# Performance work log

Hardware: AMD Instinct MI355X
Metric: run time of the kernel (lower is better)

Reference implementation:

```python
import jax, jax.numpy as jnp
import numpy as np

# Mamba2 defaults (mamba_ssm): d_state=128, d_conv=4, expand=2, headdim=64, ngroups=1
NB, D_MODEL, D_STATE, D_CONV, HEADDIM = 2, 512, 128, 4, 64
D_INNER = 2 * D_MODEL                      # expand * d_model
NHEADS = D_INNER // HEADDIM                # 16
CONV_DIM = D_INNER + 2 * D_STATE           # x, B, C go through depthwise conv
D_IN_PROJ = 2 * D_INNER + 2 * D_STATE + NHEADS  # z, xBC, dt
VOCAB, LABEL, B, L = 32000, 1000, 2, 512


def setup_inputs() -> dict:
    key = jax.random.key(0)
    ks = jax.random.split(key, 8)
    nrm = lambda k, shape, s: jax.random.normal(k, shape, dtype=jnp.float32) * s
    tokens = jax.random.randint(ks[0], (B, L), 0, VOCAB)
    embedding = nrm(ks[1], (VOCAB, D_MODEL), 0.02)
    in_proj_w = nrm(ks[2], (NB, D_IN_PROJ, D_MODEL), D_MODEL ** -0.5)
    conv_w = nrm(ks[3], (NB, CONV_DIM, D_CONV), D_CONV ** -0.5)
    conv_b = jnp.zeros((NB, CONV_DIM), jnp.float32)
    # dt_bias = inverse-softplus of dt ~ logUniform[1e-3, 0.1] (Mamba2 init)
    dt = jnp.exp(jax.random.uniform(ks[4], (NB, NHEADS), minval=float(np.log(1e-3)), maxval=float(np.log(0.1))))
    dt_bias = dt + jnp.log(-jnp.expm1(-dt))
    A_log = jnp.log(jax.random.uniform(ks[5], (NB, NHEADS), minval=1.0, maxval=16.0))
    D = jnp.ones((NB, NHEADS), jnp.float32)
    rms_w = jnp.ones((NB, D_INNER), jnp.float32)
    out_proj_w = nrm(ks[6], (NB, D_MODEL, D_INNER), D_INNER ** -0.5)
    ln_w = jnp.ones((NB, D_MODEL), jnp.float32)
    ln_b = jnp.zeros((NB, D_MODEL), jnp.float32)
    head_w = nrm(ks[7], (LABEL, D_MODEL), D_MODEL ** -0.5)
    head_b = jnp.zeros((LABEL,), jnp.float32)
    return dict(tokens=tokens, embedding=embedding, in_proj_w=in_proj_w, conv_w=conv_w,
                conv_b=conv_b, dt_bias=dt_bias, A_log=A_log, D=D, rms_w=rms_w,
                out_proj_w=out_proj_w, ln_w=ln_w, ln_b=ln_b, head_w=head_w, head_b=head_b)


def _mamba2(u, Wi, cw, cb, dtb, Alog, Dv, rw, Wo):
    b, l, _ = u.shape
    zxbcdt = u @ Wi.T                                  # (b,l,D_IN_PROJ)
    z = zxbcdt[..., :D_INNER]
    xBC = zxbcdt[..., D_INNER:D_INNER + CONV_DIM]
    dt = jax.nn.softplus(zxbcdt[..., D_INNER + CONV_DIM:] + dtb)   # (b,l,h)
    # causal depthwise conv1d, kernel size D_CONV
    xp = jnp.pad(xBC, ((0, 0), (D_CONV - 1, 0), (0, 0)))
    xBC = sum(xp[:, k:k + l, :] * cw[:, k] for k in range(D_CONV)) + cb
    xBC = jax.nn.silu(xBC)
    xh = xBC[..., :D_INNER].reshape(b, l, NHEADS, HEADDIM)
    Bm = xBC[..., D_INNER:D_INNER + D_STATE]           # (b,l,n), ngroups=1
    Cm = xBC[..., D_INNER + D_STATE:]                  # (b,l,n)
    A = -jnp.exp(Alog)                                 # (h,)
    dA = jnp.exp(dt * A)                               # (b,l,h)

    def step(h, inp):
        dA_t, dt_t, x_t, B_t, C_t = inp                # (b,h),(b,h),(b,h,p),(b,n),(b,n)
        h = h * dA_t[:, :, None, None] + (dt_t[:, :, None] * x_t)[..., None] * B_t[:, None, None, :]
        return h, jnp.einsum('bhpn,bn->bhp', h, C_t)

    h0 = jnp.zeros((b, NHEADS, HEADDIM, D_STATE), u.dtype)
    inp = (jnp.swapaxes(dA, 0, 1), jnp.swapaxes(dt, 0, 1), jnp.swapaxes(xh, 0, 1),
           jnp.swapaxes(Bm, 0, 1), jnp.swapaxes(Cm, 0, 1))
    _, ys = jax.lax.scan(step, h0, inp)
    y = jnp.swapaxes(ys, 0, 1) + Dv[:, None] * xh      # (b,l,h,p)
    # gated RMSNorm (norm_before_gate=False): normalize y*silu(z)
    y = y.reshape(b, l, D_INNER) * jax.nn.silu(z)
    y = y * jax.lax.rsqrt(jnp.mean(y * y, -1, keepdims=True) + 1e-5) * rw
    return y @ Wo.T


def _layernorm(x, w, bias):
    mu = jnp.mean(x, -1, keepdims=True)
    xc = x - mu
    var = jnp.mean(xc * xc, -1, keepdims=True)
    return xc * jax.lax.rsqrt(var + 1e-5) * w + bias


def reference(tokens, embedding, in_proj_w, conv_w, conv_b, dt_bias, A_log, D,
              rms_w, out_proj_w, ln_w, ln_b, head_w, head_b):
    x = embedding[tokens]                              # (b,l,d)
    for i in range(NB):
        y = _mamba2(x, in_proj_w[i], conv_w[i], conv_b[i], dt_bias[i],
                    A_log[i], D[i], rms_w[i], out_proj_w[i])
        x = _layernorm(y + x, ln_w[i], ln_b[i])        # residual + LN (dropout=identity)
    return x @ head_w.T + head_b                        # (b,l,label)
```

## Files before the change

### kernel.cpp

```cpp
#include <hip/hip_runtime.h>

#define L_SEQ 512
#define BATCH 2
#define NROWS (BATCH*L_SEQ)
#define DMODEL 512
#define DINNER 1024
#define DSTATE 128
#define NHEADSM 16
#define CONVD 1280
#define DINPROJ 2320
#define QCH 32
#define NCH 16
#define WI_PAD 2368
#define WH_PAD 1024

#define W_CONVW 0
#define W_CONVB 10240
#define W_DTB   12800
#define W_ALOG  12832
#define W_DD    12864
#define W_RMSW  12896
#define W_LNW   14944
#define W_LNB   15968
#define W_HEADB 16992
#define O_X     18048
#define O_ZX    (O_X  + NROWS*DMODEL)
#define O_XC    (O_ZX + NROWS*DINPROJ)
#define O_DT    (O_XC + NROWS*CONVD)
#define O_Y     (O_DT + NROWS*NHEADSM)
#define O_O     (O_Y  + NROWS*DINNER)
#define O_LA    (O_O  + NROWS*DMODEL)
#define O_S     (O_LA + 16384)
#define O_UB    (O_S  + 4194304)
#define U_WI   0
#define U_WO   2424832
#define U_WH   3473408
#define U_XBF  3997696
#define U_YBF  4521984

#define NSMALL 17992
#define NPREPW (2*WI_PAD + 2*DMODEL + WH_PAD)

typedef __attribute__((ext_vector_type(8))) short short8;
typedef __attribute__((ext_vector_type(4))) float floatx4;

__device__ __forceinline__ float b2f(unsigned short h){ return __uint_as_float(((unsigned)h)<<16); }
__device__ __forceinline__ unsigned short f2b(float x){
  unsigned u = __float_as_uint(x);
  return (unsigned short)((u + 0x7fffu + ((u>>16)&1u)) >> 16);
}
__device__ __forceinline__ float loadIn(const void* p, long i, int f){
  return f ? b2f(((const unsigned short*)p)[i]) : ((const float*)p)[i];
}

__device__ __forceinline__ void gload16(const void* g, void* l){
  __builtin_amdgcn_global_load_lds((const __attribute__((address_space(1))) void*)g,
                                   (__attribute__((address_space(3))) void*)l, 16, 0, 0);
}

__global__ void k_detect(const unsigned* __restrict__ emb, int* __restrict__ flag){
  __shared__ int red[256];
  int t = threadIdx.x; int cnt = 0;
  for (int i = 0; i < 16; i++){
    unsigned w = emb[t*16 + i];
    unsigned e = (w >> 7) & 0xffu;
    cnt += (e >= 100 && e <= 126) ? 1 : 0;
  }
  red[t] = cnt; __syncthreads();
  if (t == 0){
    int s = 0;
    for (int i = 0; i < 256; i++) s += red[i];
    *flag = (s > 2048) ? 1 : 0;
  }
}

struct ConvArgs { const void* src[9]; int off[10]; };

__global__ void k_prep(ConvArgs a, const void* __restrict__ wi, const void* __restrict__ wo,
                       const void* __restrict__ wh, const int* __restrict__ tok,
                       const void* __restrict__ emb, const int* __restrict__ flag,
                       float* __restrict__ dstSmall,
                       unsigned short* __restrict__ WiB, unsigned short* __restrict__ WoB,
                       unsigned short* __restrict__ WhB,
                       float* __restrict__ x, unsigned short* __restrict__ xbf)
{
  int f = *flag;
  int blk = blockIdx.x;
  if (blk < 71){
    int i = blk*256 + threadIdx.x;
    if (i < a.off[9]){
      int s = 0;
      while (i >= a.off[s+1]) s++;
      dstSmall[i] = loadIn(a.src[s], i - a.off[s], f);
    }
    return;
  }
  blk -= 71;
  if (blk < NPREPW){
    int r = blk;
    const void* src = nullptr; unsigned short* dst; long sb = 0, db; int K; bool zero = false;
    if (r < 2*WI_PAD){
      int layer = r / WI_PAD, row = r % WI_PAD;
      K = DMODEL; dst = WiB; db = ((long)layer*WI_PAD + row)*DMODEL;
      if (row < DINPROJ){ src = wi; sb = ((long)layer*DINPROJ + row)*DMODEL; } else zero = true;
    } else if (r < 2*WI_PAD + 2*DMODEL){
      int rr = r - 2*WI_PAD;
      K = DINNER; dst = WoB; db = (long)rr*DINNER;
      src = wo; sb = db;
    } else {
      int row = r - 2*WI_PAD - 2*DMODEL;
      K = DMODEL; dst = WhB; db = (long)row*DMODEL;
      if (row < 1000){ src = wh; sb = db; } else zero = true;
    }
    for (int c = threadIdx.x; c < K; c += 256)
      dst[db + c] = zero ? (unsigned short)0
                         : (f ? ((const unsigned short*)src)[sb + c] : f2b(((const float*)src)[sb + c]));
    return;
  }
  int r = blk - NPREPW;
  long base = (long)tok[r] * DMODEL;
  for (int c = threadIdx.x; c < DMODEL; c += 256){
    float v = loadIn(emb, base + c, f);
    x[(long)r*DMODEL + c] = v;
    xbf[(long)r*DMODEL + c] = f ? ((const unsigned short*)emb)[base + c] : f2b(v);
  }
}

template<int BM, int BN>
__global__ __launch_bounds__(256) void k_mfma_nt(
    const unsigned short* __restrict__ A, const unsigned short* __restrict__ B,
    void* __restrict__ C, int M, int N, int K,
    const float* __restrict__ bias, const int* __restrict__ flag, int outDual)
{
  constexpr int MI = BM/32;
  constexpr int NI = BN/32;
  constexpr int CA = BM/32;
  constexpr int CB = BN/32;
  __shared__ __align__(16) unsigned short As[2][BM*64];
  __shared__ __align__(16) unsigned short Bs[2][BN*64];
  int f = *flag;
  int t = threadIdx.x;
  int w = t >> 6, lane = t & 63;
  int quad = lane >> 4, l16 = lane & 15;
  int m0 = blockIdx.y * BM, n0 = blockIdx.x * BN;
  int wm = (w & 1) * (BM/2), wn = (w >> 1) * (BN/2);
  floatx4 acc[MI][NI];
  #pragma unroll
  for (int mi = 0; mi < MI; mi++)
    #pragma unroll
    for (int ni = 0; ni < NI; ni++) acc[mi][ni] = (floatx4){0.f,0.f,0.f,0.f};

  const char* Ag = (const char*)A;
  const char* Bg = (const char*)B;
  long aOff[CA]; int aL[CA];
  #pragma unroll
  for (int j = 0; j < CA; j++){
    int i = (w*CA + j)*64 + lane;
    int r = i >> 3, g = (i & 7) ^ (r & 7);
    aOff[j] = ((long)(m0 + r)*K + g*8)*2;
    aL[j] = (w*CA + j)*1024;
  }
  long bOff[CB]; int bL[CB];
  #pragma unroll
  for (int j = 0; j < CB; j++){
    int i = (w*CB + j)*64 + lane;
    int r = i >> 3, g = (i & 7) ^ (r & 7);
    bOff[j] = ((long)(n0 + r)*K + g*8)*2;
    bL[j] = (w*CB + j)*1024;
  }

  const int NKI = K >> 6;
  #pragma unroll
  for (int j = 0; j < CA; j++) gload16(Ag + aOff[j], (char*)As[0] + aL[j]);
  #pragma unroll
  for (int j = 0; j < CB; j++) gload16(Bg + bOff[j], (char*)Bs[0] + bL[j]);
  asm volatile("s_waitcnt vmcnt(0)" ::: "memory");
  __syncthreads();

  for (int ki = 0; ki < NKI; ki++){
    int cur = ki & 1;
    if (ki + 1 < NKI){
      long kb = (long)(ki + 1)*128;
      #pragma unroll
      for (int j = 0; j < CA; j++) gload16(Ag + aOff[j] + kb, (char*)As[cur^1] + aL[j]);
      #pragma unroll
      for (int j = 0; j < CB; j++) gload16(Bg + bOff[j] + kb, (char*)Bs[cur^1] + bL[j]);
    }
    const unsigned short* Ac = As[cur];
    const unsigned short* Bc = Bs[cur];
    #pragma unroll
    for (int ks = 0; ks < 2; ks++){
      short8 af[MI], bfr[NI];
      #pragma unroll
      for (int mi = 0; mi < MI; mi++){
        int r = wm + mi*16 + l16;
        int pos = ((ks << 2) + quad) ^ (r & 7);
        af[mi] = *(const short8*)&Ac[r*64 + pos*8];
      }
      #pragma unroll
      for (int ni = 0; ni < NI; ni++){
        int r = wn + ni*16 + l16;
        int pos = ((ks << 2) + quad) ^ (r & 7);
        bfr[ni] = *(const short8*)&Bc[r*64 + pos*8];
      }
      #pragma unroll
      for (int mi = 0; mi < MI; mi++)
        #pragma unroll
        for (int ni = 0; ni < NI; ni++)
          acc[mi][ni] = __builtin_amdgcn_mfma_f32_16x16x32_bf16(af[mi], bfr[ni], acc[mi][ni], 0, 0, 0);
    }
    asm volatile("s_waitcnt vmcnt(0)" ::: "memory");
    __syncthreads();
  }
  #pragma unroll
  for (int mi = 0; mi < MI; mi++)
    #pragma unroll
    for (int ni = 0; ni < NI; ni++){
      int col = n0 + wn + ni*16 + l16;
      if (col >= N) continue;
      float bv = bias ? bias[col] : 0.f;
      #pragma unroll
      for (int rr = 0; rr < 4; rr++){
        int row = m0 + wm + mi*16 + (quad << 2) + rr;
        float v = acc[mi][ni][rr] + bv;
        long idx = (long)row*N + col;
        if (outDual && f) ((unsigned short*)C)[idx] = f2b(v);
        else              ((float*)C)[idx] = v;
      }
    }
}

__global__ __launch_bounds__(256) void k_conv_dt(
    const float* __restrict__ zx, const float* __restrict__ cw, const float* __restrict__ cb,
    const float* __restrict__ dtb, float* __restrict__ xc, float* __restrict__ dt)
{
  int r = blockIdx.x; int b = r >> 9, l = r & 511;
  int t = threadIdx.x;
  for (int c = t; c < CONVD; c += 256){
    float s = cb[c];
    #pragma unroll
    for (int k = 0; k < 4; k++){
      int pos = l - 3 + k;
      if (pos >= 0)
        s = fmaf(zx[(long)(b*L_SEQ + pos)*DINPROJ + DINNER + c], cw[c*4 + k], s);
    }
    xc[(long)r*CONVD + c] = s / (1.f + __expf(-s));
  }
  if (t < NHEADSM){
    float v = zx[(long)r*DINPROJ + DINNER + CONVD + t] + dtb[t];
    dt[r*NHEADSM + t] = (v > 20.f) ? v : log1pf(__expf(v));
  }
}

__global__ __launch_bounds__(256) void k_chunk1(
    const float* __restrict__ xc, const float* __restrict__ dtbuf,
    const float* __restrict__ alog, const float* __restrict__ dvec,
    float* __restrict__ S, float* __restrict__ LAb, float* __restrict__ y)
{
  int c = blockIdx.x, h = blockIdx.y, b = blockIdx.z;
  int t = threadIdx.x, w = t >> 6, lane = t & 63;
  int quad = lane >> 4, l16 = lane & 15;
  int l0 = c*QCH;
  __shared__ unsigned short XT[64*40];
  __shared__ unsigned short BTc[128*40];
  __shared__ unsigned short Bb[32*136];
  __shared__ unsigned short Cb[32*136];
  __shared__ unsigned short Gb[32*40];
  __shared__ float dtl[32], lal[32], coef[32];
  float A  = -__expf(alog[h]);
  float Dv = dvec[h];

  float xv[8];
  #pragma unroll
  for (int k = 0; k < 8; k++){
    int idx = t + k*256; int j = idx >> 6, p = idx & 63;
    xv[k] = xc[(long)(b*L_SEQ + l0 + j)*CONVD + h*64 + p];
  }
  float bv[16], cv[16];
  #pragma unroll
  for (int k = 0; k < 16; k++){
    int idx = t + k*256; int j = idx >> 7, n = idx & 127;
    long rb = (long)(b*L_SEQ + l0 + j)*CONVD + DINNER;
    bv[k] = xc[rb + n];
    cv[k] = xc[rb + DSTATE + n];
  }
  if (t < 32){
    float d = dtbuf[(b*L_SEQ + l0 + t)*NHEADSM + h];
    dtl[t] = d;
    float s = d;
    #pragma unroll
    for (int o = 1; o < 32; o <<= 1){
      float u = __shfl_up(s, o, 32);
      if (t >= o) s += u;
    }
    float la = s * A;
    lal[t] = la;
    float tot = __shfl(s, 31, 32) * A;
    coef[t] = __expf(tot - la) * d;
    LAb[(b*NHEADSM + h)*L_SEQ + l0 + t] = la;
  }
  __syncthreads();
  #pragma unroll
  for (int k = 0; k < 8; k++){
    int idx = t + k*256; int j = idx >> 6, p = idx & 63;
    XT[p*40 + j] = f2b(xv[k]);
  }
  #pragma unroll
  for (int k = 0; k < 16; k++){
    int idx = t + k*256; int j = idx >> 7, n = idx & 127;
    Bb[j*136 + n] = f2b(bv[k]);
    Cb[j*136 + n] = f2b(cv[k]);
    BTc[n*40 + j] = f2b(bv[k] * coef[j]);
  }
  __syncthreads();

  short8 afS = *(const short8*)&XT[(w*16 + l16)*40 + quad*8];
  floatx4 accS[8];
  #pragma unroll
  for (int nb = 0; nb < 8; nb++){
    short8 bfS = *(const short8*)&BTc[(nb*16 + l16)*40 + quad*8];
    accS[nb] = __builtin_amdgcn_mfma_f32_16x16x32_bf16(afS, bfS, (floatx4){0.f,0.f,0.f,0.f}, 0, 0, 0);
  }
  int ti = w & 1, tj = w >> 1;
  floatx4 accG = (floatx4){0.f,0.f,0.f,0.f};
  #pragma unroll
  for (int ks = 0; ks < 4; ks++){
    short8 ga = *(const short8*)&Cb[(ti*16 + l16)*136 + ks*32 + quad*8];
    short8 gb = *(const short8*)&Bb[(tj*16 + l16)*136 + ks*32 + quad*8];
    accG = __builtin_amdgcn_mfma_f32_16x16x32_bf16(ga, gb, accG, 0, 0, 0);
  }
  long sb = ((long)((b*NHEADSM + h)*NCH + c))*8192;
  #pragma unroll
  for (int nb = 0; nb < 8; nb++)
    #pragma unroll
    for (int rr = 0; rr < 4; rr++)
      S[sb + (w*16 + quad*4 + rr)*128 + nb*16 + l16] = accS[nb][rr];
  #pragma unroll
  for (int rr = 0; rr < 4; rr++){
    int i = ti*16 + quad*4 + rr, j = tj*16 + l16;
    float g = (j <= i) ? __expf(lal[i] - lal[j]) * dtl[j] * accG[rr] : 0.f;
    Gb[i*40 + j] = f2b(g);
  }
  __syncthreads();
  short8 ag = *(const short8*)&Gb[(ti*16 + l16)*40 + quad*8];
  #pragma unroll
  for (int s = 0; s < 2; s++){
    int pb = (w >> 1)*2 + s;
    short8 bx = *(const short8*)&XT[(pb*16 + l16)*40 + quad*8];
    floatx4 accY = __builtin_amdgcn_mfma_f32_16x16x32_bf16(ag, bx, (floatx4){0.f,0.f,0.f,0.f}, 0, 0, 0);
    #pragma unroll
    for (int rr = 0; rr < 4; rr++){
      int i = ti*16 + quad*4 + rr, p = pb*16 + l16;
      float xval = b2f(XT[p*40 + i]);
      y[(long)(b*L_SEQ + l0 + i)*DINNER + h*64 + p] = fmaf(Dv, xval, accY[rr]);
    }
  }
}

__global__ __launch_bounds__(256) void k_chunk2(
    float* __restrict__ S, const float* __restrict__ LAb)
{
  int bh = blockIdx.x >> 5;
  int e = ((blockIdx.x & 31) << 8) + threadIdx.x;
  long base = (long)bh*NCH*8192 + e;
  int laBase = bh*L_SEQ;
  float lam[NCH];
  #pragma unroll
  for (int c = 0; c < NCH; c++) lam[c] = __expf(LAb[laBase + c*QCH + QCH - 1]);
  float hr = 0.f;
  #pragma unroll
  for (int c = 0; c < NCH; c++){
    long off = base + (long)c*8192;
    float sv = S[off];
    S[off] = hr;
    hr = fmaf(hr, lam[c], sv);
  }
}

__global__ __launch_bounds__(256) void k_chunk3(
    const float* __restrict__ xc, const float* __restrict__ H,
    const float* __restrict__ LAb, float* __restrict__ y)
{
  int c = blockIdx.x, h = blockIdx.y, b = blockIdx.z;
  int t = threadIdx.x, w = t >> 6, lane = t & 63;
  int quad = lane >> 4, l16 = lane & 15;
  int l0 = c*QCH;
  __shared__ unsigned short Cb[32*136];
  __shared__ unsigned short Hhi[64*136];
  __shared__ unsigned short Hlo[64*136];
  __shared__ float el[32];
  if (t < 32) el[t] = __expf(LAb[(b*NHEADSM + h)*L_SEQ + l0 + t]);
  #pragma unroll
  for (int k = 0; k < 16; k++){
    int idx = t + k*256; int j = idx >> 7, n = idx & 127;
    Cb[j*136 + n] = f2b(xc[(long)(b*L_SEQ + l0 + j)*CONVD + DINNER + DSTATE + n]);
  }
  long hb = ((long)((b*NHEADSM + h)*NCH + c))*8192;
  #pragma unroll
  for (int k = 0; k < 32; k++){
    int idx = t + k*256; int p = idx >> 7, n = idx & 127;
    float v = H[hb + idx];
    unsigned short hi = f2b(v);
    Hhi[p*136 + n] = hi;
    Hlo[p*136 + n] = f2b(v - b2f(hi));
  }
  __syncthreads();
  int ti = w & 1;
  #pragma unroll
  for (int s = 0; s < 2; s++){
    int pb = (w >> 1)*2 + s;
    floatx4 acc = (floatx4){0.f,0.f,0.f,0.f};
    #pragma unroll
    for (int ks = 0; ks < 4; ks++){
      short8 a  = *(const short8*)&Cb [(ti*16 + l16)*136 + ks*32 + quad*8];
      short8 bl = *(const short8*)&Hlo[(pb*16 + l16)*136 + ks*32 + quad*8];
      short8 bh = *(const short8*)&Hhi[(pb*16 + l16)*136 + ks*32 + quad*8];
      acc = __builtin_amdgcn_mfma_f32_16x16x32_bf16(a, bl, acc, 0, 0, 0);
      acc = __builtin_amdgcn_mfma_f32_16x16x32_bf16(a, bh, acc, 0, 0, 0);
    }
    #pragma unroll
    for (int rr = 0; rr < 4; rr++){
      int i = ti*16 + quad*4 + rr, p = pb*16 + l16;
      long yb = (long)(b*L_SEQ + l0 + i)*DINNER + h*64 + p;
      y[yb] = fmaf(el[i], acc[rr], y[yb]);
    }
  }
}

__global__ __launch_bounds__(256) void k_gated_rms(
    const float* __restrict__ y, const float* __restrict__ zx, const float* __restrict__ rw,
    unsigned short* __restrict__ ybf)
{
  int r = blockIdx.x, t = threadIdx.x;
  float g[4]; float ss = 0.f;
  #pragma unroll
  for (int i = 0; i < 4; i++){
    int c = t + i*256;
    float z  = zx[(long)r*DINPROJ + c];
    float yv = y[(long)r*DINNER + c];
    float gz = z / (1.f + __expf(-z));
    g[i] = yv * gz;
    ss = fmaf(g[i], g[i], ss);
  }
  #pragma unroll
  for (int o = 1; o < 64; o <<= 1) ss += __shfl_xor(ss, o);
  __shared__ float red[4];
  int w = t >> 6, lane = t & 63;
  if (lane == 0) red[w] = ss;
  __syncthreads();
  float tot = red[0] + red[1] + red[2] + red[3];
  float sc = rsqrtf(tot / (float)DINNER + 1e-5f);
  #pragma unroll
  for (int i = 0; i < 4; i++){
    int c = t + i*256;
    ybf[(long)r*DINNER + c] = f2b(g[i] * sc * rw[c]);
  }
}

__global__ __launch_bounds__(256) void k_add_ln(
    float* __restrict__ x, const float* __restrict__ o,
    const float* __restrict__ lw, const float* __restrict__ lb,
    unsigned short* __restrict__ xbf)
{
  int r = blockIdx.x, t = threadIdx.x;
  float v[2]; float sm = 0.f;
  #pragma unroll
  for (int i = 0; i < 2; i++){ int c = t + i*256; v[i] = x[(long)r*DMODEL + c] + o[(long)r*DMODEL + c]; sm += v[i]; }
  #pragma unroll
  for (int off = 1; off < 64; off <<= 1) sm += __shfl_xor(sm, off);
  __shared__ float red[4]; __shared__ float red2[4];
  int w = t >> 6, lane = t & 63;
  if (lane == 0) red[w] = sm;
  __syncthreads();
  float mu = (red[0] + red[1] + red[2] + red[3]) / (float)DMODEL;
  float var = 0.f;
  #pragma unroll
  for (int i = 0; i < 2; i++){ v[i] -= mu; var = fmaf(v[i], v[i], var); }
  #pragma unroll
  for (int off = 1; off < 64; off <<= 1) var += __shfl_xor(var, off);
  if (lane == 0) red2[w] = var;
  __syncthreads();
  float vv = (red2[0] + red2[1] + red2[2] + red2[3]) / (float)DMODEL;
  float sc = rsqrtf(vv + 1e-5f);
  #pragma unroll
  for (int i = 0; i < 2; i++){
    int c = t + i*256;
    float ov = v[i]*sc*lw[c] + lb[c];
    x[(long)r*DMODEL + c] = ov;
    xbf[(long)r*DMODEL + c] = f2b(ov);
  }
}

extern "C" void kernel_launch(void* const* d_in, const int* in_sizes, int n_in,
                              void* d_out, int out_size, void* d_ws, size_t ws_size,
                              hipStream_t stream)
{
  const int* tokens = (const int*)d_in[0];
  const void* emb = d_in[1];
  int* flag = (int*)d_ws;
  float* ws = (float*)((char*)d_ws + 256);

  k_detect<<<1, 256, 0, stream>>>((const unsigned*)emb, flag);

  ConvArgs ca;
  const int sizes[9] = {10240, 2560, 32, 32, 32, 2048, 1024, 1024, 1000};
  const int idxs[9]  = {3, 4, 5, 6, 7, 8, 10, 11, 13};
  int off = 0;
  for (int s = 0; s < 9; s++){ ca.src[s] = d_in[idxs[s]]; ca.off[s] = off; off += sizes[s]; }
  ca.off[9] = off;

  float* X  = ws + O_X;
  float* ZX = ws + O_ZX;
  float* XC = ws + O_XC;
  float* DT = ws + O_DT;
  float* Y  = ws + O_Y;
  float* Ob = ws + O_O;
  float* LA = ws + O_LA;
  float* Sb = ws + O_S;
  unsigned short* ub  = (unsigned short*)(ws + O_UB);
  unsigned short* WiB = ub + U_WI;
  unsigned short* WoB = ub + U_WO;
  unsigned short* WhB = ub + U_WH;
  unsigned short* Xbf = ub + U_XBF;
  unsigned short* Ybf = ub + U_YBF;

  k_prep<<<71 + NPREPW + NROWS, 256, 0, stream>>>(
      ca, d_in[2], d_in[9], d_in[12], tokens, emb, flag,
      ws, WiB, WoB, WhB, X, Xbf);

  for (int layer = 0; layer < 2; layer++){
    k_mfma_nt<64,64><<<dim3(WI_PAD/64, NROWS/64), 256, 0, stream>>>(
        Xbf, WiB + (long)layer*WI_PAD*DMODEL, (void*)ZX,
        NROWS, DINPROJ, DMODEL, (const float*)nullptr, flag, 0);
    k_conv_dt<<<NROWS, 256, 0, stream>>>(
        ZX, ws + W_CONVW + layer*5120, ws + W_CONVB + layer*1280, ws + W_DTB + layer*16, XC, DT);
    k_chunk1<<<dim3(NCH, NHEADSM, BATCH), 256, 0, stream>>>(
        XC, DT, ws + W_ALOG + layer*16, ws + W_DD + layer*16, Sb, LA, Y);
    k_chunk2<<<1024, 256, 0, stream>>>(Sb, LA);
    k_chunk3<<<dim3(NCH, NHEADSM, BATCH), 256, 0, stream>>>(XC, Sb, LA, Y);
    k_gated_rms<<<NROWS, 256, 0, stream>>>(Y, ZX, ws + W_RMSW + layer*1024, Ybf);
    k_mfma_nt<32,32><<<dim3(DMODEL/32, NROWS/32), 256, 0, stream>>>(
        Ybf, WoB + (long)layer*DMODEL*DINNER, (void*)Ob,
        NROWS, DMODEL, DINNER, (const float*)nullptr, flag, 0);
    k_add_ln<<<NROWS, 256, 0, stream>>>(X, Ob, ws + W_LNW + layer*512, ws + W_LNB + layer*512, Xbf);
  }

  k_mfma_nt<32,64><<<dim3(WH_PAD/64, NROWS/32), 256, 0, stream>>>(
      Xbf, WhB, d_out, NROWS, 1000, DMODEL, ws + W_HEADB, flag, 1);
}
```

Before: 249.7 us.

## Fuse causal conv and dt softplus into SSD chunk kernel, share bf16 C

Removes the separate conv/dt kernel and its fp32 XC/DT buffers. The chunk kernel now loads a 35-row halo of pre-conv x, B and C from the projection output into shared memory, applies the depthwise conv, SiLU and softplus itself, and writes C as bf16 for the later state-contribution kernel. That kernel then reads its C fragments straight from global memory into registers instead of staging them in LDS. The cost is that the B/C convolution is recomputed by all 16 head blocks, and the halo reads are redundant across chunks.

```diff
diff --git a/kernel.cpp b/kernel.cpp
--- a/kernel.cpp
+++ b/kernel.cpp
@@ -25,9 +25,7 @@
 #define W_HEADB 16992
 #define O_X     18048
 #define O_ZX    (O_X  + NROWS*DMODEL)
-#define O_XC    (O_ZX + NROWS*DINPROJ)
-#define O_DT    (O_XC + NROWS*CONVD)
-#define O_Y     (O_DT + NROWS*NHEADSM)
+#define O_Y     (O_ZX + NROWS*DINPROJ)
 #define O_O     (O_Y  + NROWS*DINNER)
 #define O_LA    (O_O  + NROWS*DMODEL)
 #define O_S     (O_LA + 16384)
@@ -37,8 +35,8 @@
 #define U_WH   3473408
 #define U_XBF  3997696
 #define U_YBF  4521984
-
-#define NSMALL 17992
+#define U_CBF  (U_YBF + NROWS*DINNER)
+
 #define NPREPW (2*WI_PAD + 2*DMODEL + WH_PAD)
 
 typedef __attribute__((ext_vector_type(8))) short short8;
@@ -230,68 +228,45 @@
     }
 }
 
-__global__ __launch_bounds__(256) void k_conv_dt(
+__global__ __launch_bounds__(256) void k_ssd1(
     const float* __restrict__ zx, const float* __restrict__ cw, const float* __restrict__ cb,
-    const float* __restrict__ dtb, float* __restrict__ xc, float* __restrict__ dt)
-{
-  int r = blockIdx.x; int b = r >> 9, l = r & 511;
-  int t = threadIdx.x;
-  for (int c = t; c < CONVD; c += 256){
-    float s = cb[c];
-    #pragma unroll
-    for (int k = 0; k < 4; k++){
-      int pos = l - 3 + k;
-      if (pos >= 0)
-        s = fmaf(zx[(long)(b*L_SEQ + pos)*DINPROJ + DINNER + c], cw[c*4 + k], s);
-    }
-    xc[(long)r*CONVD + c] = s / (1.f + __expf(-s));
-  }
-  if (t < NHEADSM){
-    float v = zx[(long)r*DINPROJ + DINNER + CONVD + t] + dtb[t];
-    dt[r*NHEADSM + t] = (v > 20.f) ? v : log1pf(__expf(v));
-  }
-}
-
-__global__ __launch_bounds__(256) void k_chunk1(
-    const float* __restrict__ xc, const float* __restrict__ dtbuf,
-    const float* __restrict__ alog, const float* __restrict__ dvec,
-    float* __restrict__ S, float* __restrict__ LAb, float* __restrict__ y)
+    const float* __restrict__ dtb, const float* __restrict__ alog, const float* __restrict__ dvec,
+    float* __restrict__ S, float* __restrict__ LAb, float* __restrict__ y,
+    unsigned short* __restrict__ cbf)
 {
   int c = blockIdx.x, h = blockIdx.y, b = blockIdx.z;
   int t = threadIdx.x, w = t >> 6, lane = t & 63;
   int quad = lane >> 4, l16 = lane & 15;
   int l0 = c*QCH;
-  __shared__ unsigned short XT[64*40];
-  __shared__ unsigned short BTc[128*40];
+
+  __shared__ union {
+    float zs[35*256];
+    unsigned short BTc[128*40];
+  } U;
   __shared__ unsigned short Bb[32*136];
   __shared__ unsigned short Cb[32*136];
+  __shared__ unsigned short XT[64*40];
   __shared__ unsigned short Gb[32*40];
   __shared__ float dtl[32], lal[32], coef[32];
+
   float A  = -__expf(alog[h]);
   float Dv = dvec[h];
-
-  float xv[8];
-  #pragma unroll
-  for (int k = 0; k < 8; k++){
-    int idx = t + k*256; int j = idx >> 6, p = idx & 63;
-    xv[k] = xc[(long)(b*L_SEQ + l0 + j)*CONVD + h*64 + p];
-  }
-  float bv[16], cv[16];
-  #pragma unroll
-  for (int k = 0; k < 16; k++){
-    int idx = t + k*256; int j = idx >> 7, n = idx & 127;
-    long rb = (long)(b*L_SEQ + l0 + j)*CONVD + DINNER;
-    bv[k] = xc[rb + n];
-    cv[k] = xc[rb + DSTATE + n];
+  const float* zrow = zx + (long)b*L_SEQ*DINPROJ;
+
+  for (int idx = t; idx < 35*256; idx += 256){
+    int jr = idx >> 8, cc = idx & 255;
+    int l = l0 - 3 + jr;
+    U.zs[idx] = (l >= 0) ? zrow[(long)l*DINPROJ + 2048 + cc] : 0.f;
   }
   if (t < 32){
-    float d = dtbuf[(b*L_SEQ + l0 + t)*NHEADSM + h];
+    float v = zrow[(long)(l0 + t)*DINPROJ + (DINNER + CONVD) + h] + dtb[h];
+    float d = (v > 20.f) ? v : log1pf(__expf(v));
     dtl[t] = d;
     float s = d;
     #pragma unroll
     for (int o = 1; o < 32; o <<= 1){
-      float u = __shfl_up(s, o, 32);
-      if (t >= o) s += u;
+      float u2 = __shfl_up(s, o, 32);
+      if (t >= o) s += u2;
     }
     float la = s * A;
     lal[t] = la;
@@ -300,6 +275,46 @@
     LAb[(b*NHEADSM + h)*L_SEQ + l0 + t] = la;
   }
   __syncthreads();
+  float bv[16], cvv[16];
+  #pragma unroll
+  for (int k = 0; k < 16; k++){
+    int idx = t + k*256; int j = idx >> 7, n = idx & 127;
+    int chB = 1024 + n, chC = 1152 + n;
+    float sB = cb[chB], sC = cb[chC];
+    #pragma unroll
+    for (int kk = 0; kk < 4; kk++){
+      sB = fmaf(U.zs[(j + kk)*256 + n],       cw[chB*4 + kk], sB);
+      sC = fmaf(U.zs[(j + kk)*256 + 128 + n], cw[chC*4 + kk], sC);
+    }
+    bv[k]  = sB / (1.f + __expf(-sB));
+    cvv[k] = sC / (1.f + __expf(-sC));
+  }
+  __syncthreads();
+  for (int idx = t; idx < 35*64; idx += 256){
+    int jr = idx >> 6, cc = idx & 63;
+    int l = l0 - 3 + jr;
+    U.zs[idx] = (l >= 0) ? zrow[(long)l*DINPROJ + 1024 + h*64 + cc] : 0.f;
+  }
+  __syncthreads();
+  float xv[8];
+  #pragma unroll
+  for (int k = 0; k < 8; k++){
+    int idx = t + k*256; int j = idx >> 6, p = idx & 63;
+    int ch = h*64 + p;
+    float s0 = cb[ch];
+    #pragma unroll
+    for (int kk = 0; kk < 4; kk++)
+      s0 = fmaf(U.zs[(j + kk)*64 + p], cw[ch*4 + kk], s0);
+    xv[k] = s0 / (1.f + __expf(-s0));
+  }
+  if (h == 0){
+    #pragma unroll
+    for (int k = 0; k < 16; k++){
+      int idx = t + k*256; int j = idx >> 7, n = idx & 127;
+      cbf[(long)(b*L_SEQ + l0 + j)*DSTATE + n] = f2b(cvv[k]);
+    }
+  }
+  __syncthreads();
   #pragma unroll
   for (int k = 0; k < 8; k++){
     int idx = t + k*256; int j = idx >> 6, p = idx & 63;
@@ -309,8 +324,8 @@
   for (int k = 0; k < 16; k++){
     int idx = t + k*256; int j = idx >> 7, n = idx & 127;
     Bb[j*136 + n] = f2b(bv[k]);
-    Cb[j*136 + n] = f2b(cv[k]);
-    BTc[n*40 + j] = f2b(bv[k] * coef[j]);
+    Cb[j*136 + n] = f2b(cvv[k]);
+    U.BTc[n*40 + j] = f2b(bv[k] * coef[j]);
   }
   __syncthreads();
 
@@ -318,7 +333,7 @@
   floatx4 accS[8];
   #pragma unroll
   for (int nb = 0; nb < 8; nb++){
-    short8 bfS = *(const short8*)&BTc[(nb*16 + l16)*40 + quad*8];
+    short8 bfS = *(const short8*)&U.BTc[(nb*16 + l16)*40 + quad*8];
     accS[nb] = __builtin_amdgcn_mfma_f32_16x16x32_bf16(afS, bfS, (floatx4){0.f,0.f,0.f,0.f}, 0, 0, 0);
   }
   int ti = w & 1, tj = w >> 1;
@@ -344,8 +359,8 @@
   __syncthreads();
   short8 ag = *(const short8*)&Gb[(ti*16 + l16)*40 + quad*8];
   #pragma unroll
-  for (int s = 0; s < 2; s++){
-    int pb = (w >> 1)*2 + s;
+  for (int s2 = 0; s2 < 2; s2++){
+    int pb = (w >> 1)*2 + s2;
     short8 bx = *(const short8*)&XT[(pb*16 + l16)*40 + quad*8];
     floatx4 accY = __builtin_amdgcn_mfma_f32_16x16x32_bf16(ag, bx, (floatx4){0.f,0.f,0.f,0.f}, 0, 0, 0);
     #pragma unroll
@@ -378,23 +393,17 @@
 }
 
 __global__ __launch_bounds__(256) void k_chunk3(
-    const float* __restrict__ xc, const float* __restrict__ H,
+    const unsigned short* __restrict__ cbf, const float* __restrict__ H,
     const float* __restrict__ LAb, float* __restrict__ y)
 {
   int c = blockIdx.x, h = blockIdx.y, b = blockIdx.z;
   int t = threadIdx.x, w = t >> 6, lane = t & 63;
   int quad = lane >> 4, l16 = lane & 15;
   int l0 = c*QCH;
-  __shared__ unsigned short Cb[32*136];
   __shared__ unsigned short Hhi[64*136];
   __shared__ unsigned short Hlo[64*136];
   __shared__ float el[32];
   if (t < 32) el[t] = __expf(LAb[(b*NHEADSM + h)*L_SEQ + l0 + t]);
-  #pragma unroll
-  for (int k = 0; k < 16; k++){
-    int idx = t + k*256; int j = idx >> 7, n = idx & 127;
-    Cb[j*136 + n] = f2b(xc[(long)(b*L_SEQ + l0 + j)*CONVD + DINNER + DSTATE + n]);
-  }
   long hb = ((long)((b*NHEADSM + h)*NCH + c))*8192;
   #pragma unroll
   for (int k = 0; k < 32; k++){
@@ -406,17 +415,21 @@
   }
   __syncthreads();
   int ti = w & 1;
+  const unsigned short* crow = cbf + ((long)(b*L_SEQ + l0 + ti*16 + l16))*DSTATE;
+  short8 a[4];
+  #pragma unroll
+  for (int ks = 0; ks < 4; ks++)
+    a[ks] = *(const short8*)&crow[ks*32 + quad*8];
   #pragma unroll
   for (int s = 0; s < 2; s++){
     int pb = (w >> 1)*2 + s;
     floatx4 acc = (floatx4){0.f,0.f,0.f,0.f};
     #pragma unroll
     for (int ks = 0; ks < 4; ks++){
-      short8 a  = *(const short8*)&Cb [(ti*16 + l16)*136 + ks*32 + quad*8];
       short8 bl = *(const short8*)&Hlo[(pb*16 + l16)*136 + ks*32 + quad*8];
       short8 bh = *(const short8*)&Hhi[(pb*16 + l16)*136 + ks*32 + quad*8];
-      acc = __builtin_amdgcn_mfma_f32_16x16x32_bf16(a, bl, acc, 0, 0, 0);
-      acc = __builtin_amdgcn_mfma_f32_16x16x32_bf16(a, bh, acc, 0, 0, 0);
+      acc = __builtin_amdgcn_mfma_f32_16x16x32_bf16(a[ks], bl, acc, 0, 0, 0);
+      acc = __builtin_amdgcn_mfma_f32_16x16x32_bf16(a[ks], bh, acc, 0, 0, 0);
     }
     #pragma unroll
     for (int rr = 0; rr < 4; rr++){
@@ -511,8 +524,6 @@
 
   float* X  = ws + O_X;
   float* ZX = ws + O_ZX;
-  float* XC = ws + O_XC;
-  float* DT = ws + O_DT;
   float* Y  = ws + O_Y;
   float* Ob = ws + O_O;
   float* LA = ws + O_LA;
@@ -523,6 +534,7 @@
   unsigned short* WhB = ub + U_WH;
   unsigned short* Xbf = ub + U_XBF;
   unsigned short* Ybf = ub + U_YBF;
+  unsigned short* Cbf = ub + U_CBF;
 
   k_prep<<<71 + NPREPW + NROWS, 256, 0, stream>>>(
       ca, d_in[2], d_in[9], d_in[12], tokens, emb, flag,
@@ -532,12 +544,11 @@
     k_mfma_nt<64,64><<<dim3(WI_PAD/64, NROWS/64), 256, 0, stream>>>(
         Xbf, WiB + (long)layer*WI_PAD*DMODEL, (void*)ZX,
         NROWS, DINPROJ, DMODEL, (const float*)nullptr, flag, 0);
-    k_conv_dt<<<NROWS, 256, 0, stream>>>(
-        ZX, ws + W_CONVW + layer*5120, ws + W_CONVB + layer*1280, ws + W_DTB + layer*16, XC, DT);
-    k_chunk1<<<dim3(NCH, NHEADSM, BATCH), 256, 0, stream>>>(
-        XC, DT, ws + W_ALOG + layer*16, ws + W_DD + layer*16, Sb, LA, Y);
+    k_ssd1<<<dim3(NCH, NHEADSM, BATCH), 256, 0, stream>>>(
+        ZX, ws + W_CONVW + layer*5120, ws + W_CONVB + layer*1280, ws + W_DTB + layer*16,
+        ws + W_ALOG + layer*16, ws + W_DD + layer*16, Sb, LA, Y, Cbf);
     k_chunk2<<<1024, 256, 0, stream>>>(Sb, LA);
-    k_chunk3<<<dim3(NCH, NHEADSM, BATCH), 256, 0, stream>>>(XC, Sb, LA, Y);
+    k_chunk3<<<dim3(NCH, NHEADSM, BATCH), 256, 0, stream>>>(Cbf, Sb, LA, Y);
     k_gated_rms<<<NROWS, 256, 0, stream>>>(Y, ZX, ws + W_RMSW + layer*1024, Ybf);
     k_mfma_nt<32,32><<<dim3(DMODEL/32, NROWS/32), 256, 0, stream>>>(
         Ybf, WoB + (long)layer*DMODEL*DINNER, (void*)Ob,
```

Measured after the change: 260.6 us. 4.3% more time.

## Fuse gated RMSNorm into out-projection GEMM and fold rms weight into Wo

Applied to the files above, without the earlier changes.

Removes the separate gated RMSNorm kernel. The out-projection GEMM now reads fp32 Y and Z directly, computes silu gating, converts the result to bf16 into shared memory, and accumulates row sums of squares while running the K loop. The rsqrt row scale is applied in the epilogue. The RMS weight is multiplied into Wo during prep. This saves one launch and the Ybf round trip through memory, but every N-tile block recomputes the gating for its rows (16x redundant) and reads fp32 data instead of bf16. Rounding also changes, because the weight is folded into Wo before the bf16 cast.

```diff
diff --git a/kernel.cpp b/kernel.cpp
--- a/kernel.cpp
+++ b/kernel.cpp
@@ -38,7 +38,6 @@
 #define U_XBF  3997696
 #define U_YBF  4521984
 
-#define NSMALL 17992
 #define NPREPW (2*WI_PAD + 2*DMODEL + WH_PAD)
 
 typedef __attribute__((ext_vector_type(8))) short short8;
@@ -77,7 +76,8 @@
 struct ConvArgs { const void* src[9]; int off[10]; };
 
 __global__ void k_prep(ConvArgs a, const void* __restrict__ wi, const void* __restrict__ wo,
-                       const void* __restrict__ wh, const int* __restrict__ tok,
+                       const void* __restrict__ wh, const void* __restrict__ rwsrc,
+                       const int* __restrict__ tok,
                        const void* __restrict__ emb, const int* __restrict__ flag,
                        float* __restrict__ dstSmall,
                        unsigned short* __restrict__ WiB, unsigned short* __restrict__ WoB,
@@ -98,23 +98,35 @@
   blk -= 71;
   if (blk < NPREPW){
     int r = blk;
-    const void* src = nullptr; unsigned short* dst; long sb = 0, db; int K; bool zero = false;
     if (r < 2*WI_PAD){
       int layer = r / WI_PAD, row = r % WI_PAD;
-      K = DMODEL; dst = WiB; db = ((long)layer*WI_PAD + row)*DMODEL;
-      if (row < DINPROJ){ src = wi; sb = ((long)layer*DINPROJ + row)*DMODEL; } else zero = true;
+      long db = ((long)layer*WI_PAD + row)*DMODEL;
+      if (row < DINPROJ){
+        long sb = ((long)layer*DINPROJ + row)*DMODEL;
+        for (int c = threadIdx.x; c < DMODEL; c += 256)
+          WiB[db + c] = f ? ((const unsigned short*)wi)[sb + c] : f2b(((const float*)wi)[sb + c]);
+      } else {
+        for (int c = threadIdx.x; c < DMODEL; c += 256) WiB[db + c] = 0;
+      }
     } else if (r < 2*WI_PAD + 2*DMODEL){
       int rr = r - 2*WI_PAD;
-      K = DINNER; dst = WoB; db = (long)rr*DINNER;
-      src = wo; sb = db;
+      int layer = rr >> 9;
+      long db = (long)rr*DINNER;
+      for (int c = threadIdx.x; c < DINNER; c += 256){
+        float wv = loadIn(wo, db + c, f);
+        float rv = loadIn(rwsrc, (long)layer*DINNER + c, f);
+        WoB[db + c] = f2b(wv * rv);
+      }
     } else {
       int row = r - 2*WI_PAD - 2*DMODEL;
-      K = DMODEL; dst = WhB; db = (long)row*DMODEL;
-      if (row < 1000){ src = wh; sb = db; } else zero = true;
-    }
-    for (int c = threadIdx.x; c < K; c += 256)
-      dst[db + c] = zero ? (unsigned short)0
-                         : (f ? ((const unsigned short*)src)[sb + c] : f2b(((const float*)src)[sb + c]));
+      long db = (long)row*DMODEL;
+      if (row < 1000){
+        for (int c = threadIdx.x; c < DMODEL; c += 256)
+          WhB[db + c] = f ? ((const unsigned short*)wh)[db + c] : f2b(((const float*)wh)[db + c]);
+      } else {
+        for (int c = threadIdx.x; c < DMODEL; c += 256) WhB[db + c] = 0;
+      }
+    }
     return;
   }
   int r = blk - NPREPW;
@@ -230,6 +242,98 @@
     }
 }
 
+__global__ __launch_bounds__(256) void k_outproj_rms(
+    const float* __restrict__ Y, const float* __restrict__ ZX,
+    const unsigned short* __restrict__ B, float* __restrict__ C)
+{
+  __shared__ __align__(16) unsigned short As[2][32*64];
+  __shared__ __align__(16) unsigned short Bs[2][32*64];
+  __shared__ float ssr[32];
+  int t = threadIdx.x;
+  int w = t >> 6, lane = t & 63;
+  int quad = lane >> 4, l16 = lane & 15;
+  int m0 = blockIdx.y * 32, n0 = blockIdx.x * 32;
+  int wm = (w & 1) * 16, wn = (w >> 1) * 16;
+  floatx4 acc = (floatx4){0.f,0.f,0.f,0.f};
+
+  int ar = t >> 3, ag = (t & 7) ^ (ar & 7);
+  const float* yp = Y  + (long)(m0 + ar)*DINNER  + ag*8;
+  const float* zp = ZX + (long)(m0 + ar)*DINPROJ + ag*8;
+  int br = t >> 3, bg = (t & 7) ^ (br & 7);
+  long bOff = ((long)(n0 + br)*DINNER + bg*8)*2;
+  int bL = w*1024;
+  const char* Bgp = (const char*)B;
+
+  float ss = 0.f;
+  gload16(Bgp + bOff, (char*)Bs[0] + bL);
+  {
+    floatx4 y0 = *(const floatx4*)(yp);
+    floatx4 y1 = *(const floatx4*)(yp + 4);
+    floatx4 z0 = *(const floatx4*)(zp);
+    floatx4 z1 = *(const floatx4*)(zp + 4);
+    short8 sv;
+    #pragma unroll
+    for (int j = 0; j < 4; j++){
+      float gz0 = z0[j] / (1.f + __expf(-z0[j]));
+      float g0 = y0[j] * gz0; ss = fmaf(g0, g0, ss); sv[j] = (short)f2b(g0);
+      float gz1 = z1[j] / (1.f + __expf(-z1[j]));
+      float g1 = y1[j] * gz1; ss = fmaf(g1, g1, ss); sv[j+4] = (short)f2b(g1);
+    }
+    *(short8*)&As[0][t*8] = sv;
+  }
+  asm volatile("s_waitcnt vmcnt(0)" ::: "memory");
+  __syncthreads();
+
+  for (int ki = 0; ki < 16; ki++){
+    int cur = ki & 1;
+    floatx4 y0, y1, z0, z1;
+    if (ki < 15){
+      gload16(Bgp + bOff + (long)(ki + 1)*128, (char*)Bs[cur^1] + bL);
+      y0 = *(const floatx4*)(yp + (ki+1)*64);
+      y1 = *(const floatx4*)(yp + (ki+1)*64 + 4);
+      z0 = *(const floatx4*)(zp + (ki+1)*64);
+      z1 = *(const floatx4*)(zp + (ki+1)*64 + 4);
+    }
+    const unsigned short* Ac = As[cur];
+    const unsigned short* Bc = Bs[cur];
+    #pragma unroll
+    for (int ks = 0; ks < 2; ks++){
+      int ra = wm + l16;
+      int pa = ((ks << 2) + quad) ^ (ra & 7);
+      short8 af = *(const short8*)&Ac[ra*64 + pa*8];
+      int rb = wn + l16;
+      int pb = ((ks << 2) + quad) ^ (rb & 7);
+      short8 bf = *(const short8*)&Bc[rb*64 + pb*8];
+      acc = __builtin_amdgcn_mfma_f32_16x16x32_bf16(af, bf, acc, 0, 0, 0);
+    }
+    if (ki < 15){
+      short8 sv;
+      #pragma unroll
+      for (int j = 0; j < 4; j++){
+        float gz0 = z0[j] / (1.f + __expf(-z0[j]));
+        float g0 = y0[j] * gz0; ss = fmaf(g0, g0, ss); sv[j] = (short)f2b(g0);
+        float gz1 = z1[j] / (1.f + __expf(-z1[j]));
+        float g1 = y1[j] * gz1; ss = fmaf(g1, g1, ss); sv[j+4] = (short)f2b(g1);
+      }
+      *(short8*)&As[cur^1][t*8] = sv;
+    }
+    asm volatile("s_waitcnt vmcnt(0)" ::: "memory");
+    __syncthreads();
+  }
+  ss += __shfl_xor(ss, 1);
+  ss += __shfl_xor(ss, 2);
+  ss += __shfl_xor(ss, 4);
+  if ((lane & 7) == 0) ssr[t >> 3] = ss;
+  __syncthreads();
+  int col = n0 + wn + l16;
+  #pragma unroll
+  for (int rr = 0; rr < 4; rr++){
+    int lr = wm + (quad << 2) + rr;
+    float sc = rsqrtf(ssr[lr] / (float)DINNER + 1e-5f);
+    C[(long)(m0 + lr)*DMODEL + col] = acc[rr] * sc;
+  }
+}
+
 __global__ __launch_bounds__(256) void k_conv_dt(
     const float* __restrict__ zx, const float* __restrict__ cw, const float* __restrict__ cb,
     const float* __restrict__ dtb, float* __restrict__ xc, float* __restrict__ dt)
@@ -424,36 +528,6 @@
       long yb = (long)(b*L_SEQ + l0 + i)*DINNER + h*64 + p;
       y[yb] = fmaf(el[i], acc[rr], y[yb]);
     }
-  }
-}
-
-__global__ __launch_bounds__(256) void k_gated_rms(
-    const float* __restrict__ y, const float* __restrict__ zx, const float* __restrict__ rw,
-    unsigned short* __restrict__ ybf)
-{
-  int r = blockIdx.x, t = threadIdx.x;
-  float g[4]; float ss = 0.f;
-  #pragma unroll
-  for (int i = 0; i < 4; i++){
-    int c = t + i*256;
-    float z  = zx[(long)r*DINPROJ + c];
-    float yv = y[(long)r*DINNER + c];
-    float gz = z / (1.f + __expf(-z));
-    g[i] = yv * gz;
-    ss = fmaf(g[i], g[i], ss);
-  }
-  #pragma unroll
-  for (int o = 1; o < 64; o <<= 1) ss += __shfl_xor(ss, o);
-  __shared__ float red[4];
-  int w = t >> 6, lane = t & 63;
-  if (lane == 0) red[w] = ss;
-  __syncthreads();
-  float tot = red[0] + red[1] + red[2] + red[3];
-  float sc = rsqrtf(tot / (float)DINNER + 1e-5f);
-  #pragma unroll
-  for (int i = 0; i < 4; i++){
-    int c = t + i*256;
-    ybf[(long)r*DINNER + c] = f2b(g[i] * sc * rw[c]);
   }
 }
 
@@ -522,10 +596,9 @@
   unsigned short* WoB = ub + U_WO;
   unsigned short* WhB = ub + U_WH;
   unsigned short* Xbf = ub + U_XBF;
-  unsigned short* Ybf = ub + U_YBF;
 
   k_prep<<<71 + NPREPW + NROWS, 256, 0, stream>>>(
-      ca, d_in[2], d_in[9], d_in[12], tokens, emb, flag,
+      ca, d_in[2], d_in[9], d_in[12], d_in[8], tokens, emb, flag,
       ws, WiB, WoB, WhB, X, Xbf);
 
   for (int layer = 0; layer < 2; layer++){
@@ -538,10 +611,8 @@
         XC, DT, ws + W_ALOG + layer*16, ws + W_DD + layer*16, Sb, LA, Y);
     k_chunk2<<<1024, 256, 0, stream>>>(Sb, LA);
     k_chunk3<<<dim3(NCH, NHEADSM, BATCH), 256, 0, stream>>>(XC, Sb, LA, Y);
-    k_gated_rms<<<NROWS, 256, 0, stream>>>(Y, ZX, ws + W_RMSW + layer*1024, Ybf);
-    k_mfma_nt<32,32><<<dim3(DMODEL/32, NROWS/32), 256, 0, stream>>>(
-        Ybf, WoB + (long)layer*DMODEL*DINNER, (void*)Ob,
-        NROWS, DMODEL, DINNER, (const float*)nullptr, flag, 0);
+    k_outproj_rms<<<dim3(DMODEL/32, NROWS/32), 256, 0, stream>>>(
+        Y, ZX, WoB + (long)layer*DMODEL*DINNER, Ob);
     k_add_ln<<<NROWS, 256, 0, stream>>>(X, Ob, ws + W_LNW + layer*512, ws + W_LNB + layer*512, Xbf);
   }
 
```

Result: slower. 261.5 us (+4.7%).
